# Optimization experiments

Hardware: AMD Instinct MI355X
Metric: run time of the kernel (lower is better)

## Reference

```python
import jax, jax.numpy as jnp
import numpy as np
from jax import lax

WIN = 7
PAD = WIN // 2
K1, K2 = 0.01, 0.03
NP = WIN * WIN
COV_NORM = NP / (NP - 1)  # use_sample_covariance=True


def _dwconv(x, w, channel):
    # depthwise 2D conv, SAME-style explicit padding (torch conv2d padding=pad)
    return lax.conv_general_dilated(
        x, w, window_strides=(1, 1),
        padding=[(PAD, PAD), (PAD, PAD)],
        feature_group_count=channel,
        dimension_numbers=('NCHW', 'OIHW', 'NCHW'))


def setup_inputs() -> dict:
    key = jax.random.key(0)
    k1, k2 = jax.random.split(key)
    B, C, H, W = 64, 1, 384, 384
    gt = jax.random.uniform(k1, (B, C, H, W), dtype=jnp.float32)
    pred = jax.random.uniform(k2, (B, C, H, W), dtype=jnp.float32)
    # uniform (box) window: create_window(7, channel=1, gaussian_weights=False)
    window = jnp.ones((C, 1, WIN, WIN), dtype=jnp.float32) / NP
    return {"gt": gt, "pred": pred, "window": window}


def reference(gt, pred, window):
    channel = gt.shape[1]
    data_range = jnp.max(gt)  # data_range=None default

    ux = _dwconv(gt, window, channel)
    uy = _dwconv(pred, window, channel)
    uxx = _dwconv(gt * gt, window, channel) - ux * ux
    uyy = _dwconv(pred * pred, window, channel) - uy * uy
    uxy = _dwconv(gt * pred, window, channel) - ux * uy

    vx = COV_NORM * uxx
    vy = COV_NORM * uyy
    vxy = COV_NORM * uxy

    C1 = (K1 * data_range) ** 2
    C2 = (K2 * data_range) ** 2

    S = (2.0 * ux * uy + C1) * (2.0 * vxy + C2) / ((ux * ux + uy * uy + C1) * (vx + vy + C2))
    ssim_map = S[:, :, PAD:-PAD, PAD:-PAD]
    return jnp.mean(ssim_map)  # size_average=True, full=False
```

## Files before the change

### kernel.cpp

```cpp
#include <hip/hip_runtime.h>


#define PADW 3
#define BT 64
#define BAND 15
#define NCHUNK 3

constexpr int B_ = 64, H_ = 384, W_ = 384;
constexpr int W2 = W_ / 2;
constexpr int OUTD = W_ - 2 * PADW;
constexpr int NBANDS = (OUTD + BAND - 1) / BAND;
constexpr int NTILES = 3;
constexpr int TOTAL_BLOCKS = NTILES * NBANDS * B_;
constexpr double NPIX = (double)B_ * OUTD * OUTD;

__device__ __forceinline__ unsigned enc_f(float f) {
    unsigned u = __float_as_uint(f);
    return (u & 0x80000000u) ? ~u : (u | 0x80000000u);
}
__device__ __forceinline__ float dec_f(unsigned e) {
    return __uint_as_float((e & 0x80000000u) ? (e & 0x7fffffffu) : ~e);
}

__device__ __forceinline__ float2 f2add(float2 a, float2 b) { return make_float2(a.x + b.x, a.y + b.y); }
__device__ __forceinline__ float2 f2sub(float2 a, float2 b) { return make_float2(a.x - b.x, a.y - b.y); }

__global__ void __launch_bounds__(256)
max_kernel(const float4* __restrict__ g4, unsigned* ws_max, int n4) {
    int tid = blockIdx.x * blockDim.x + threadIdx.x;
    int stride = gridDim.x * blockDim.x;
    float m = -3.402823466e38f;
    for (int i = tid; i < n4; i += stride) {
        float4 v = g4[i];
        m = fmaxf(m, fmaxf(fmaxf(v.x, v.y), fmaxf(v.z, v.w)));
    }
#pragma unroll
    for (int off = 32; off > 0; off >>= 1)
        m = fmaxf(m, __shfl_down(m, off));
    __shared__ float sm[4];
    if ((threadIdx.x & 63) == 0) sm[threadIdx.x >> 6] = m;
    __syncthreads();
    if (threadIdx.x == 0) {
        float mm = fmaxf(fmaxf(sm[0], sm[1]), fmaxf(sm[2], sm[3]));
        atomicMax(ws_max, enc_f(mm));
    }
}

__device__ __forceinline__ float ssim_px(float sx, float sy, float sxx, float syy, float sxy,
                                         float C1, float C2) {
    const float inv49 = 1.0f / 49.0f;
    const float covn  = 49.0f / 48.0f;
    float ux  = sx * inv49, uy = sy * inv49;
    float uxx = sxx * inv49 - ux * ux;
    float uyy = syy * inv49 - uy * uy;
    float uxy = sxy * inv49 - ux * uy;
    float vvx = covn * uxx, vvy = covn * uyy, vvxy = covn * uxy;
    float num = (2.0f * ux * uy + C1) * (2.0f * vvxy + C2);
    float den = (ux * ux + uy * uy + C1) * (vvx + vvy + C2);
    return num / den;
}

__global__ void __launch_bounds__(BT)
ssim_kernel(const float* __restrict__ gt, const float* __restrict__ pred,
            const unsigned* __restrict__ ws_max, double* __restrict__ ws_part) {
    const int t    = threadIdx.x;
    const int tile = blockIdx.x;
    const int band = blockIdx.y;
    const int b    = blockIdx.z;
    const int bid  = (b * NBANDS + band) * NTILES + tile;

    const float dr = dec_f(*ws_max);
    const float C1 = (0.01f * dr) * (0.01f * dr);
    const float C2 = (0.03f * dr) * (0.03f * dr);

    const int  row0   = band * BAND;
    const int  cbase2 = tile * 63;
    const bool active = (t < 63);

    __shared__ float2 sg[7][68];
    __shared__ float2 sp[7][68];

    float2 rx[7], ry[7], rxx[7], ryy[7], rxy[7];
#pragma unroll
    for (int j = 0; j < 7; ++j) {
        rx[j] = make_float2(0.f, 0.f); ry[j] = rx[j];
        rxx[j] = rx[j]; ryy[j] = rx[j]; rxy[j] = rx[j];
    }
    float2 vx = make_float2(0.f, 0.f), vy = vx, vxx = vx, vyy = vx, vxy = vx;
    double acc = 0.0;

    const float2* gbase = (const float2*)(gt   + (size_t)b * H_ * W_);
    const float2* pbase = (const float2*)(pred + (size_t)b * H_ * W_);

    for (int c = 0; c < NCHUNK; ++c) {
        __syncthreads();
#pragma unroll
        for (int j = 0; j < 7; ++j) {
            const int ir = min(row0 + c * 7 + j, H_ - 1);
            const float2* gr = gbase + (size_t)ir * W2 + cbase2;
            const float2* pr = pbase + (size_t)ir * W2 + cbase2;
            sg[j][t] = gr[t];
            sp[j][t] = pr[t];
            if (t < 2) {
                sg[j][64 + t] = gr[64 + t];
                sp[j][64 + t] = pr[64 + t];
            }
        }
        __syncthreads();

#pragma unroll
        for (int j = 0; j < 7; ++j) {
            float2 d0 = sg[j][t], d1 = sg[j][t + 1], d2 = sg[j][t + 2], d3 = sg[j][t + 3];
            float2 e0 = sp[j][t], e1 = sp[j][t + 1], e2 = sp[j][t + 2], e3 = sp[j][t + 3];

            float hx0 = d0.x + d0.y + d1.x + d1.y + d2.x + d2.y + d3.x;
            float hy0 = e0.x + e0.y + e1.x + e1.y + e2.x + e2.y + e3.x;
            float hxx0 = fmaf(d0.x, d0.x, fmaf(d0.y, d0.y, fmaf(d1.x, d1.x,
                         fmaf(d1.y, d1.y, fmaf(d2.x, d2.x, fmaf(d2.y, d2.y, d3.x * d3.x))))));
            float hyy0 = fmaf(e0.x, e0.x, fmaf(e0.y, e0.y, fmaf(e1.x, e1.x,
                         fmaf(e1.y, e1.y, fmaf(e2.x, e2.x, fmaf(e2.y, e2.y, e3.x * e3.x))))));
            float hxy0 = fmaf(d0.x, e0.x, fmaf(d0.y, e0.y, fmaf(d1.x, e1.x,
                         fmaf(d1.y, e1.y, fmaf(d2.x, e2.x, fmaf(d2.y, e2.y, d3.x * e3.x))))));

            float2 h_x  = make_float2(hx0,  hx0  - d0.x        + d3.y);
            float2 h_y  = make_float2(hy0,  hy0  - e0.x        + e3.y);
            float2 h_xx = make_float2(hxx0, hxx0 - d0.x * d0.x + d3.y * d3.y);
            float2 h_yy = make_float2(hyy0, hyy0 - e0.x * e0.x + e3.y * e3.y);
            float2 h_xy = make_float2(hxy0, hxy0 - d0.x * e0.x + d3.y * e3.y);

            vx  = f2add(vx,  f2sub(h_x,  rx[j]));  rx[j]  = h_x;
            vy  = f2add(vy,  f2sub(h_y,  ry[j]));  ry[j]  = h_y;
            vxx = f2add(vxx, f2sub(h_xx, rxx[j])); rxx[j] = h_xx;
            vyy = f2add(vyy, f2sub(h_yy, ryy[j])); ryy[j] = h_yy;
            vxy = f2add(vxy, f2sub(h_xy, rxy[j])); rxy[j] = h_xy;

            const int i = c * 7 + j;
            if (i >= 6) {
                const int orow = row0 + i - 6;
                if (active && orow < OUTD) {
                    acc += (double)ssim_px(vx.x, vy.x, vxx.x, vyy.x, vxy.x, C1, C2)
                         + (double)ssim_px(vx.y, vy.y, vxx.y, vyy.y, vxy.y, C1, C2);
                }
            }
        }
    }

#pragma unroll
    for (int off = 32; off > 0; off >>= 1)
        acc += __shfl_down(acc, off);
    if (t == 0) ws_part[bid] = acc;
}

__global__ void __launch_bounds__(256)
final_kernel(const double* __restrict__ ws_part, float* __restrict__ out) {
    const int t = threadIdx.x;
    double s = 0.0;
    for (int i = t; i < TOTAL_BLOCKS; i += 256) s += ws_part[i];
#pragma unroll
    for (int off = 32; off > 0; off >>= 1)
        s += __shfl_down(s, off);
    __shared__ double sd[4];
    if ((t & 63) == 0) sd[t >> 6] = s;
    __syncthreads();
    if (t == 0) out[0] = (float)((sd[0] + sd[1] + sd[2] + sd[3]) / NPIX);
}

extern "C" void kernel_launch(void* const* d_in, const int* in_sizes, int n_in,
                              void* d_out, int out_size, void* d_ws, size_t ws_size,
                              hipStream_t stream) {
    const float* gt   = (const float*)d_in[0];
    const float* pred = (const float*)d_in[1];
    float* out = (float*)d_out;

    unsigned* ws_max  = (unsigned*)d_ws;
    double*   ws_part = (double*)((char*)d_ws + 64);

    hipMemsetAsync(d_ws, 0, 64, stream);

    const int n4 = B_ * H_ * W_ / 4;
    max_kernel<<<1024, 256, 0, stream>>>((const float4*)gt, ws_max, n4);

    dim3 grid(NTILES, NBANDS, B_);
    ssim_kernel<<<grid, BT, 0, stream>>>(gt, pred, ws_max, ws_part);

    final_kernel<<<1, 256, 0, stream>>>(ws_part, out);
}
```

Before: 158.1 us.

## Switch SSIM kernel to one pixel per thread with more column tiles

Each thread now handles a single output column instead of a float2 pair, so the grid uses twice as many column tiles and shared memory holds scalar floats. The horizontal 7-tap sums are recomputed directly rather than shared across the pair, per-chunk results go into a float accumulator before widening to double, and the division becomes a hardware reciprocal. The aim is more parallelism and fewer double-precision adds, paid for with more shared-memory reads, duplicated halo loads across tiles, and slightly lower precision in the division.

```diff
diff --git a/kernel.cpp b/kernel.cpp
--- a/kernel.cpp
+++ b/kernel.cpp
@@ -3,14 +3,14 @@
 
 #define PADW 3
 #define BT 64
+#define TILEC 63
 #define BAND 15
 #define NCHUNK 3
 
 constexpr int B_ = 64, H_ = 384, W_ = 384;
-constexpr int W2 = W_ / 2;
 constexpr int OUTD = W_ - 2 * PADW;
 constexpr int NBANDS = (OUTD + BAND - 1) / BAND;
-constexpr int NTILES = 3;
+constexpr int NTILES = 6;
 constexpr int TOTAL_BLOCKS = NTILES * NBANDS * B_;
 constexpr double NPIX = (double)B_ * OUTD * OUTD;
 
@@ -21,9 +21,6 @@
 __device__ __forceinline__ float dec_f(unsigned e) {
     return __uint_as_float((e & 0x80000000u) ? (e & 0x7fffffffu) : ~e);
 }
-
-__device__ __forceinline__ float2 f2add(float2 a, float2 b) { return make_float2(a.x + b.x, a.y + b.y); }
-__device__ __forceinline__ float2 f2sub(float2 a, float2 b) { return make_float2(a.x - b.x, a.y - b.y); }
 
 __global__ void __launch_bounds__(256)
 max_kernel(const float4* __restrict__ g4, unsigned* ws_max, int n4) {
@@ -57,7 +54,7 @@
     float vvx = covn * uxx, vvy = covn * uyy, vvxy = covn * uxy;
     float num = (2.0f * ux * uy + C1) * (2.0f * vvxy + C2);
     float den = (ux * ux + uy * uy + C1) * (vvx + vvy + C2);
-    return num / den;
+    return num * __builtin_amdgcn_rcpf(den);
 }
 
 __global__ void __launch_bounds__(BT)
@@ -73,76 +70,64 @@
     const float C1 = (0.01f * dr) * (0.01f * dr);
     const float C2 = (0.03f * dr) * (0.03f * dr);
 
-    const int  row0   = band * BAND;
-    const int  cbase2 = tile * 63;
-    const bool active = (t < 63);
+    const int row0 = band * BAND;
+    const int cb   = tile * TILEC;
 
-    __shared__ float2 sg[7][68];
-    __shared__ float2 sp[7][68];
+    __shared__ float sg[7][72];
+    __shared__ float sp[7][72];
 
-    float2 rx[7], ry[7], rxx[7], ryy[7], rxy[7];
+    float rx[7], ry[7], rxx[7], ryy[7], rxy[7];
 #pragma unroll
-    for (int j = 0; j < 7; ++j) {
-        rx[j] = make_float2(0.f, 0.f); ry[j] = rx[j];
-        rxx[j] = rx[j]; ryy[j] = rx[j]; rxy[j] = rx[j];
-    }
-    float2 vx = make_float2(0.f, 0.f), vy = vx, vxx = vx, vyy = vx, vxy = vx;
+    for (int j = 0; j < 7; ++j) { rx[j]=0.f; ry[j]=0.f; rxx[j]=0.f; ryy[j]=0.f; rxy[j]=0.f; }
+
+    float vx = 0.f, vy = 0.f, vxx = 0.f, vyy = 0.f, vxy = 0.f;
     double acc = 0.0;
 
-    const float2* gbase = (const float2*)(gt   + (size_t)b * H_ * W_);
-    const float2* pbase = (const float2*)(pred + (size_t)b * H_ * W_);
+    const float* gbase = gt   + (size_t)b * H_ * W_;
+    const float* pbase = pred + (size_t)b * H_ * W_;
 
     for (int c = 0; c < NCHUNK; ++c) {
         __syncthreads();
 #pragma unroll
         for (int j = 0; j < 7; ++j) {
             const int ir = min(row0 + c * 7 + j, H_ - 1);
-            const float2* gr = gbase + (size_t)ir * W2 + cbase2;
-            const float2* pr = pbase + (size_t)ir * W2 + cbase2;
+            const float* gr = gbase + (size_t)ir * W_ + cb;
+            const float* pr = pbase + (size_t)ir * W_ + cb;
             sg[j][t] = gr[t];
             sp[j][t] = pr[t];
-            if (t < 2) {
+            if (t < 5) {
                 sg[j][64 + t] = gr[64 + t];
                 sp[j][64 + t] = pr[64 + t];
             }
         }
         __syncthreads();
 
+        float cpart = 0.f;
 #pragma unroll
         for (int j = 0; j < 7; ++j) {
-            float2 d0 = sg[j][t], d1 = sg[j][t + 1], d2 = sg[j][t + 2], d3 = sg[j][t + 3];
-            float2 e0 = sp[j][t], e1 = sp[j][t + 1], e2 = sp[j][t + 2], e3 = sp[j][t + 3];
-
-            float hx0 = d0.x + d0.y + d1.x + d1.y + d2.x + d2.y + d3.x;
-            float hy0 = e0.x + e0.y + e1.x + e1.y + e2.x + e2.y + e3.x;
-            float hxx0 = fmaf(d0.x, d0.x, fmaf(d0.y, d0.y, fmaf(d1.x, d1.x,
-                         fmaf(d1.y, d1.y, fmaf(d2.x, d2.x, fmaf(d2.y, d2.y, d3.x * d3.x))))));
-            float hyy0 = fmaf(e0.x, e0.x, fmaf(e0.y, e0.y, fmaf(e1.x, e1.x,
-                         fmaf(e1.y, e1.y, fmaf(e2.x, e2.x, fmaf(e2.y, e2.y, e3.x * e3.x))))));
-            float hxy0 = fmaf(d0.x, e0.x, fmaf(d0.y, e0.y, fmaf(d1.x, e1.x,
-                         fmaf(d1.y, e1.y, fmaf(d2.x, e2.x, fmaf(d2.y, e2.y, d3.x * e3.x))))));
-
-            float2 h_x  = make_float2(hx0,  hx0  - d0.x        + d3.y);
-            float2 h_y  = make_float2(hy0,  hy0  - e0.x        + e3.y);
-            float2 h_xx = make_float2(hxx0, hxx0 - d0.x * d0.x + d3.y * d3.y);
-            float2 h_yy = make_float2(hyy0, hyy0 - e0.x * e0.x + e3.y * e3.y);
-            float2 h_xy = make_float2(hxy0, hxy0 - d0.x * e0.x + d3.y * e3.y);
-
-            vx  = f2add(vx,  f2sub(h_x,  rx[j]));  rx[j]  = h_x;
-            vy  = f2add(vy,  f2sub(h_y,  ry[j]));  ry[j]  = h_y;
-            vxx = f2add(vxx, f2sub(h_xx, rxx[j])); rxx[j] = h_xx;
-            vyy = f2add(vyy, f2sub(h_yy, ryy[j])); ryy[j] = h_yy;
-            vxy = f2add(vxy, f2sub(h_xy, rxy[j])); rxy[j] = h_xy;
+            float hx = 0.f, hy = 0.f, hxx = 0.f, hyy = 0.f, hxy = 0.f;
+#pragma unroll
+            for (int k = 0; k < 7; ++k) {
+                float g = sg[j][t + k], p = sp[j][t + k];
+                hx += g; hy += p;
+                hxx = fmaf(g, g, hxx);
+                hyy = fmaf(p, p, hyy);
+                hxy = fmaf(g, p, hxy);
+            }
+            vx  += hx  - rx[j];   rx[j]  = hx;
+            vy  += hy  - ry[j];   ry[j]  = hy;
+            vxx += hxx - rxx[j];  rxx[j] = hxx;
+            vyy += hyy - ryy[j];  ryy[j] = hyy;
+            vxy += hxy - rxy[j];  rxy[j] = hxy;
 
             const int i = c * 7 + j;
             if (i >= 6) {
                 const int orow = row0 + i - 6;
-                if (active && orow < OUTD) {
-                    acc += (double)ssim_px(vx.x, vy.x, vxx.x, vyy.x, vxy.x, C1, C2)
-                         + (double)ssim_px(vx.y, vy.y, vxx.y, vyy.y, vxy.y, C1, C2);
-                }
+                if (t < TILEC && orow < OUTD)
+                    cpart += ssim_px(vx, vy, vxx, vyy, vxy, C1, C2);
             }
         }
+        acc += (double)cpart;
     }
 
 #pragma unroll
```

Result: slower. 172.3 us (+9.0%).

## Double-buffer SSIM row chunks with direct global-to-LDS async loads

Applied to the files above, without the earlier changes.

Replaces the register-staged global-to-shared copies with `__builtin_amdgcn_global_load_lds` DMA loads into LDS. Two LDS buffers are used so the next 7-row chunk is fetched while the current one is computed. The per-chunk `__syncthreads` barriers are dropped, which is safe only because each block is a single 64-thread wave. The goal is to hide global memory latency and save VGPR round trips. Correctness depends on the compiler inserting the proper vmcnt waits before LDS reads, and the overlapping loads do not fill the last float2 column, which only inactive lanes read.

```diff
diff --git a/kernel.cpp b/kernel.cpp
--- a/kernel.cpp
+++ b/kernel.cpp
@@ -24,6 +24,12 @@
 
 __device__ __forceinline__ float2 f2add(float2 a, float2 b) { return make_float2(a.x + b.x, a.y + b.y); }
 __device__ __forceinline__ float2 f2sub(float2 a, float2 b) { return make_float2(a.x - b.x, a.y - b.y); }
+
+__device__ __forceinline__ void glds4(const float* g, float* l) {
+    __builtin_amdgcn_global_load_lds(
+        (const __attribute__((address_space(1))) void*)g,
+        (__attribute__((address_space(3))) void*)l, 4, 0, 0);
+}
 
 __global__ void __launch_bounds__(256)
 max_kernel(const float4* __restrict__ g4, unsigned* ws_max, int n4) {
@@ -77,8 +83,8 @@
     const int  cbase2 = tile * 63;
     const bool active = (t < 63);
 
-    __shared__ float2 sg[7][68];
-    __shared__ float2 sp[7][68];
+    __shared__ float2 sgA[7][67], spA[7][67];
+    __shared__ float2 sgB[7][67], spB[7][67];
 
     float2 rx[7], ry[7], rxx[7], ryy[7], rxy[7];
 #pragma unroll
@@ -92,22 +98,25 @@
     const float2* gbase = (const float2*)(gt   + (size_t)b * H_ * W_);
     const float2* pbase = (const float2*)(pred + (size_t)b * H_ * W_);
 
-    for (int c = 0; c < NCHUNK; ++c) {
-        __syncthreads();
+    auto stage = [&](float2 (*dg)[67], float2 (*dp)[67], int c) {
+        const int r0 = row0 + c * 7;
 #pragma unroll
         for (int j = 0; j < 7; ++j) {
-            const int ir = min(row0 + c * 7 + j, H_ - 1);
-            const float2* gr = gbase + (size_t)ir * W2 + cbase2;
-            const float2* pr = pbase + (size_t)ir * W2 + cbase2;
-            sg[j][t] = gr[t];
-            sp[j][t] = pr[t];
-            if (t < 2) {
-                sg[j][64 + t] = gr[64 + t];
-                sp[j][64 + t] = pr[64 + t];
-            }
+            const int ir = min(r0 + j, H_ - 1);
+            const float* grf = (const float*)(gbase + (size_t)ir * W2 + cbase2);
+            const float* prf = (const float*)(pbase + (size_t)ir * W2 + cbase2);
+            float* lg = (float*)&dg[j][0];
+            float* lp = (float*)&dp[j][0];
+            glds4(grf + t,      lg + t);
+            glds4(grf + 64 + t, lg + 64 + t);
+            glds4(grf + 68 + t, lg + 68 + t);
+            glds4(prf + t,      lp + t);
+            glds4(prf + 64 + t, lp + 64 + t);
+            glds4(prf + 68 + t, lp + 68 + t);
         }
-        __syncthreads();
-
+    };
+
+    auto compute = [&](const float2 (*sg)[67], const float2 (*sp)[67], int c) {
 #pragma unroll
         for (int j = 0; j < 7; ++j) {
             float2 d0 = sg[j][t], d1 = sg[j][t + 1], d2 = sg[j][t + 2], d3 = sg[j][t + 3];
@@ -143,7 +152,14 @@
                 }
             }
         }
-    }
+    };
+
+    stage(sgA, spA, 0);
+    stage(sgB, spB, 1);
+    compute(sgA, spA, 0);
+    stage(sgA, spA, 2);
+    compute(sgB, spB, 1);
+    compute(sgA, spA, 2);
 
 #pragma unroll
     for (int off = 32; off > 0; off >>= 1)
```

New measurement: 145.2 us. -8.1%, faster.
